# Kernel tuning notes

Measured on AMD Instinct MI355X. Metric: run time of the kernel, lower is better.

The kernel has to match this reference:

```python
import jax, jax.numpy as jnp
import numpy as np

HIDDEN = 2048
INPUT = 2048
BATCH = 4096


def setup_inputs() -> dict:
    key = jax.random.key(0)
    ks = jax.random.split(key, 7)
    x = jax.random.normal(ks[0], (BATCH, INPUT), dtype=jnp.float32)
    h = jax.random.normal(ks[1], (BATCH, HIDDEN), dtype=jnp.float32)
    c = jax.random.normal(ks[2], (BATCH, HIDDEN), dtype=jnp.float32)
    # learned parameters (RandomNormal init stddev=0.05 analogue; scale irrelevant for correctness)
    w_ih = jax.random.normal(ks[3], (4, INPUT, HIDDEN), dtype=jnp.float32) * 0.05
    w_hh = jax.random.normal(ks[4], (4, HIDDEN, HIDDEN), dtype=jnp.float32) * 0.05
    b_ih = jax.random.normal(ks[5], (4, HIDDEN), dtype=jnp.float32) * 0.05
    b_hh = jax.random.normal(ks[6], (4, HIDDEN), dtype=jnp.float32) * 0.05
    return {"x": x, "h": h, "c": c, "w_ih": w_ih, "w_hh": w_hh, "b_ih": b_ih, "b_hh": b_hh}


def reference(x, h, c, w_ih, w_hh, b_ih, b_hh):
    # gates: [4, B, H] = x @ w_ih[g] and h @ w_hh[g], batched over gate dim g
    gates = (
        jnp.einsum("bi,gih->gbh", x, w_ih)
        + jnp.einsum("bh,ghk->gbk", h, w_hh)
        + (b_ih + b_hh)[:, None, :]
    )
    ingate = jax.nn.sigmoid(gates[0])
    forgetgate = jax.nn.sigmoid(gates[1])
    cellgate = jnp.tanh(gates[2])
    outgate = jax.nn.sigmoid(gates[3])
    c_new = forgetgate * c + ingate * cellgate
    h_new = outgate * jnp.tanh(c_new)
    return (h_new, c_new)
```

## Files before the change

kernel.cpp:

```cpp
#include <hip/hip_runtime.h>

#define BATCH  4096
#define HIDDEN 2048
#define INPUT  2048
#define KDIM   4096
#define NDIM   8192
#define BM 128
#define BN 128
#define BK 32

typedef __attribute__((ext_vector_type(8))) short short8;
typedef __attribute__((ext_vector_type(4))) float float4v;


__device__ __forceinline__ unsigned short f2bf(float f) {
    union { float f; unsigned u; } v; v.f = f;
    unsigned r = v.u + 0x7FFFu + ((v.u >> 16) & 1u);
    return (unsigned short)(r >> 16);
}

__device__ __forceinline__ void gl2lds16(const unsigned short* g, unsigned short* l) {
    __builtin_amdgcn_global_load_lds(
        (const __attribute__((address_space(1))) unsigned int*)g,
        (__attribute__((address_space(3))) unsigned int*)l,
        16, 0, 0);
}

__device__ __forceinline__ float sigm(float x) {
    return 1.0f / (1.0f + __expf(-x));
}
__device__ __forceinline__ float tanh_fast(float x) {
    return 2.0f / (1.0f + __expf(-2.0f * x)) - 1.0f;
}


__global__ void pack_x_kernel(const float* __restrict__ x, const float* __restrict__ h,
                              unsigned short* __restrict__ Xb) {
    int idx = blockIdx.x * 256 + threadIdx.x;
    int b  = idx >> 9;
    int ko = idx & 511;
    const float* src = (ko < 256) ? (x + (size_t)b * INPUT  + (size_t)ko * 8)
                                  : (h + (size_t)b * HIDDEN + (size_t)(ko - 256) * 8);
    float4 v0 = *(const float4*)(src);
    float4 v1 = *(const float4*)(src + 4);
    union { unsigned short us[8]; uint4 v; } o;
    o.us[0] = f2bf(v0.x); o.us[1] = f2bf(v0.y); o.us[2] = f2bf(v0.z); o.us[3] = f2bf(v0.w);
    o.us[4] = f2bf(v1.x); o.us[5] = f2bf(v1.y); o.us[6] = f2bf(v1.z); o.us[7] = f2bf(v1.w);
    *(uint4*)(Xb + (size_t)b * KDIM + (size_t)ko * 8) = o.v;
}


__global__ void pack_w_kernel(const float* __restrict__ w_ih, const float* __restrict__ w_hh,
                              unsigned short* __restrict__ Wt) {
    __shared__ unsigned short tile[32][136];
    const int k0 = blockIdx.x * 128;
    const int j0 = blockIdx.y * 32;
    const int g  = blockIdx.z;
    const float* src = (k0 < INPUT)
        ? (w_ih + (size_t)g * INPUT  * HIDDEN + (size_t)k0 * HIDDEN + j0)
        : (w_hh + (size_t)g * HIDDEN * HIDDEN + (size_t)(k0 - INPUT) * HIDDEN + j0);

    const int tid = threadIdx.x;
    const int jl  = (tid & 7) * 4;
    const int kl  = (tid >> 3) * 2;
#pragma unroll
    for (int p = 0; p < 2; ++p) {
        const int k = kl + p * 64;
        float4 v0 = *(const float4*)(src + (size_t)k * HIDDEN + jl);
        float4 v1 = *(const float4*)(src + (size_t)(k + 1) * HIDDEN + jl);
        unsigned p0 = (unsigned)f2bf(v0.x) | ((unsigned)f2bf(v1.x) << 16);
        unsigned p1 = (unsigned)f2bf(v0.y) | ((unsigned)f2bf(v1.y) << 16);
        unsigned p2 = (unsigned)f2bf(v0.z) | ((unsigned)f2bf(v1.z) << 16);
        unsigned p3 = (unsigned)f2bf(v0.w) | ((unsigned)f2bf(v1.w) << 16);
        *(unsigned*)&tile[jl + 0][k] = p0;
        *(unsigned*)&tile[jl + 1][k] = p1;
        *(unsigned*)&tile[jl + 2][k] = p2;
        *(unsigned*)&tile[jl + 3][k] = p3;
    }
    __syncthreads();

#pragma unroll
    for (int p = 0; p < 2; ++p) {
        const int c  = tid + p * 256;
        const int j  = c >> 4;
        const int k8 = c & 15;
        uint4 v = *(const uint4*)&tile[j][k8 * 8];
        *(uint4*)(Wt + (size_t)(4 * (j0 + j) + g) * KDIM + k0 + k8 * 8) = v;
    }
}


__global__ __launch_bounds__(256, 2)
void gemm_kernel(const unsigned short* __restrict__ A,
                 const unsigned short* __restrict__ B,
                 const float* __restrict__ c,
                 const float* __restrict__ b_ih,
                 const float* __restrict__ b_hh,
                 float* __restrict__ out) {
    __shared__ unsigned short As[BM * BK];
    __shared__ unsigned short Bs[BN * BK];

    const int tid  = threadIdx.x;
    const int m0   = blockIdx.y * BM;
    const int n0   = blockIdx.x * BN;
    const int wave = tid >> 6;
    const int lane = tid & 63;
    const int ln   = lane & 15;
    const int kq   = lane >> 4;
    const int wm   = (wave >> 1) * 64;
    const int wn   = (wave & 1) * 64;

    const int s0 = tid, s1 = tid + 256;
    const unsigned short* gA0 = A + (size_t)(m0 + (s0 >> 2)) * KDIM + (s0 & 3) * 8;
    const unsigned short* gA1 = A + (size_t)(m0 + (s1 >> 2)) * KDIM + (s1 & 3) * 8;
    const unsigned short* gB0 = B + (size_t)(n0 + (s0 >> 2)) * KDIM + (s0 & 3) * 8;
    const unsigned short* gB1 = B + (size_t)(n0 + (s1 >> 2)) * KDIM + (s1 & 3) * 8;
    unsigned short* lA0 = As + s0 * 8;
    unsigned short* lA1 = As + s1 * 8;
    unsigned short* lB0 = Bs + s0 * 8;
    unsigned short* lB1 = Bs + s1 * 8;

    float4v acc[4][4];
#pragma unroll
    for (int i = 0; i < 4; ++i)
#pragma unroll
        for (int j = 0; j < 4; ++j)
            acc[i][j] = (float4v){0.f, 0.f, 0.f, 0.f};

    const int a_off = (wm + ln) * BK + kq * 8;
    const int b_off = (wn + ln) * BK + kq * 8;

    for (int kt = 0; kt < KDIM / BK; ++kt) {
        const int ko = kt * BK;
        gl2lds16(gA0 + ko, lA0);
        gl2lds16(gA1 + ko, lA1);
        gl2lds16(gB0 + ko, lB0);
        gl2lds16(gB1 + ko, lB1);
        __syncthreads();

        short8 af[4], bfr[4];
#pragma unroll
        for (int mi = 0; mi < 4; ++mi)
            af[mi] = *(const short8*)(As + a_off + mi * 16 * BK);
#pragma unroll
        for (int ni = 0; ni < 4; ++ni)
            bfr[ni] = *(const short8*)(Bs + b_off + ni * 16 * BK);

#pragma unroll
        for (int mi = 0; mi < 4; ++mi)
#pragma unroll
            for (int ni = 0; ni < 4; ++ni)
                acc[mi][ni] = __builtin_amdgcn_mfma_f32_16x16x32_bf16(
                    af[mi], bfr[ni], acc[mi][ni], 0, 0, 0);

        __syncthreads();
    }

    const int q = lane & 3;
    const int t = (lane & 15) >> 2;
    const size_t HB = (size_t)BATCH * HIDDEN;

#pragma unroll
    for (int ni = 0; ni < 4; ++ni) {
        const int jg = ((n0 + wn + ni * 16) >> 2) + t;
        const float b0 = b_ih[jg]              + b_hh[jg];
        const float b1 = b_ih[HIDDEN + jg]     + b_hh[HIDDEN + jg];
        const float b2 = b_ih[2 * HIDDEN + jg] + b_hh[2 * HIDDEN + jg];
        const float b3 = b_ih[3 * HIDDEN + jg] + b_hh[3 * HIDDEN + jg];
#pragma unroll
        for (int mi = 0; mi < 4; ++mi) {
            float4v v = acc[mi][ni];
            float t1 = __shfl_xor((q & 1) ? v[0] : v[1], 1);
            float t2 = __shfl_xor((q & 1) ? v[2] : v[3], 1);
            v[0] = (q & 1) ? t1 : v[0];
            v[1] = (q & 1) ? v[1] : t1;
            v[2] = (q & 1) ? t2 : v[2];
            v[3] = (q & 1) ? v[3] : t2;
            float t3 = __shfl_xor((q & 2) ? v[0] : v[2], 2);
            float t4 = __shfl_xor((q & 2) ? v[1] : v[3], 2);
            v[0] = (q & 2) ? t3 : v[0];
            v[1] = (q & 2) ? t4 : v[1];
            v[2] = (q & 2) ? v[2] : t3;
            v[3] = (q & 2) ? v[3] : t4;

            const int row = m0 + wm + mi * 16 + kq * 4 + q;
            const float ig = sigm(v[0] + b0);
            const float fg = sigm(v[1] + b1);
            const float cg = tanh_fast(v[2] + b2);
            const float og = sigm(v[3] + b3);
            const float cv = c[(size_t)row * HIDDEN + jg];
            const float cn = fg * cv + ig * cg;
            const float hn = og * tanh_fast(cn);
            out[(size_t)row * HIDDEN + jg] = hn;
            out[HB + (size_t)row * HIDDEN + jg] = cn;
        }
    }
}


extern "C" void kernel_launch(void* const* d_in, const int* in_sizes, int n_in,
                              void* d_out, int out_size, void* d_ws, size_t ws_size,
                              hipStream_t stream) {
    const float* x    = (const float*)d_in[0];
    const float* h    = (const float*)d_in[1];
    const float* c    = (const float*)d_in[2];
    const float* w_ih = (const float*)d_in[3];
    const float* w_hh = (const float*)d_in[4];
    const float* b_ih = (const float*)d_in[5];
    const float* b_hh = (const float*)d_in[6];
    float* out = (float*)d_out;

    const size_t XB_BYTES = (size_t)BATCH * KDIM * 2;
    unsigned short* Xb = (unsigned short*)d_ws;
    unsigned short* Wt = (unsigned short*)((char*)d_ws + XB_BYTES);

    hipLaunchKernelGGL(pack_x_kernel, dim3((size_t)BATCH * KDIM / 8 / 256), dim3(256), 0, stream,
                       x, h, Xb);
    hipLaunchKernelGGL(pack_w_kernel, dim3(KDIM / 128, HIDDEN / 32, 4), dim3(256), 0, stream,
                       w_ih, w_hh, Wt);
    hipLaunchKernelGGL(gemm_kernel, dim3(NDIM / BN, BATCH / BM), dim3(256), 0, stream,
                       Xb, Wt, c, b_ih, b_hh, out);
}
```

Baseline: 565.5 us.

## Enlarge GEMM tiles to 256x256x64 with double-buffered swizzled LDS pipeline

Measured after the change: 512.7 us. -9.3%, faster.

```diff
diff --git a/kernel.cpp b/kernel.cpp
--- a/kernel.cpp
+++ b/kernel.cpp
@@ -5,9 +5,10 @@
 #define INPUT  2048
 #define KDIM   4096
 #define NDIM   8192
-#define BM 128
-#define BN 128
-#define BK 32
+#define BM 256
+#define BN 256
+#define BK 64
+#define NT (KDIM / BK)
 
 typedef __attribute__((ext_vector_type(8))) short short8;
 typedef __attribute__((ext_vector_type(4))) float float4v;
@@ -31,6 +32,12 @@
 }
 __device__ __forceinline__ float tanh_fast(float x) {
     return 2.0f / (1.0f + __expf(-2.0f * x)) - 1.0f;
+}
+
+__device__ __forceinline__ void fence_bar() {
+    asm volatile("" ::: "memory");
+    __builtin_amdgcn_s_barrier();
+    asm volatile("" ::: "memory");
 }
 
 
@@ -81,109 +88,174 @@
 
 #pragma unroll
     for (int p = 0; p < 2; ++p) {
-        const int c  = tid + p * 256;
-        const int j  = c >> 4;
-        const int k8 = c & 15;
+        const int cch = tid + p * 256;
+        const int j   = cch >> 4;
+        const int k8  = cch & 15;
         uint4 v = *(const uint4*)&tile[j][k8 * 8];
         *(uint4*)(Wt + (size_t)(4 * (j0 + j) + g) * KDIM + k0 + k8 * 8) = v;
     }
 }
 
 
-__global__ __launch_bounds__(256, 2)
+__global__ __launch_bounds__(512, 2)
 void gemm_kernel(const unsigned short* __restrict__ A,
                  const unsigned short* __restrict__ B,
                  const float* __restrict__ c,
                  const float* __restrict__ b_ih,
                  const float* __restrict__ b_hh,
                  float* __restrict__ out) {
-    __shared__ unsigned short As[BM * BK];
-    __shared__ unsigned short Bs[BN * BK];
+    extern __shared__ unsigned short lds[];
+    unsigned short* cA = lds;
+    unsigned short* nA = lds + 16384;
+    unsigned short* cB = lds + 32768;
+    unsigned short* nB = lds + 49152;
 
     const int tid  = threadIdx.x;
-    const int m0   = blockIdx.y * BM;
-    const int n0   = blockIdx.x * BN;
-    const int wave = tid >> 6;
+    const int wid  = tid >> 6;
     const int lane = tid & 63;
     const int ln   = lane & 15;
     const int kq   = lane >> 4;
-    const int wm   = (wave >> 1) * 64;
-    const int wn   = (wave & 1) * 64;
-
-    const int s0 = tid, s1 = tid + 256;
-    const unsigned short* gA0 = A + (size_t)(m0 + (s0 >> 2)) * KDIM + (s0 & 3) * 8;
-    const unsigned short* gA1 = A + (size_t)(m0 + (s1 >> 2)) * KDIM + (s1 & 3) * 8;
-    const unsigned short* gB0 = B + (size_t)(n0 + (s0 >> 2)) * KDIM + (s0 & 3) * 8;
-    const unsigned short* gB1 = B + (size_t)(n0 + (s1 >> 2)) * KDIM + (s1 & 3) * 8;
-    unsigned short* lA0 = As + s0 * 8;
-    unsigned short* lA1 = As + s1 * 8;
-    unsigned short* lB0 = Bs + s0 * 8;
-    unsigned short* lB1 = Bs + s1 * 8;
-
-    float4v acc[4][4];
-#pragma unroll
-    for (int i = 0; i < 4; ++i)
+    const int wmr  = (wid >> 2) * 128;
+    const int wnr  = (wid & 3) * 64;
+    const int m0   = blockIdx.y * BM;
+    const int n0   = blockIdx.x * BN;
+
+    const int srow  = tid >> 3;
+    const int scol8 = (tid & 7) ^ (srow & 7);
+    const unsigned short* gA[4];
+    const unsigned short* gB[4];
+#pragma unroll
+    for (int cN = 0; cN < 4; ++cN) {
+        gA[cN] = A + (size_t)(m0 + cN * 64 + srow) * KDIM + scol8 * 8;
+        gB[cN] = B + (size_t)(n0 + cN * 64 + srow) * KDIM + scol8 * 8;
+    }
+    const int dOff = tid * 8;
+
+    const int abase = (wmr + ln) * 64;
+    const int bbase = (wnr + ln) * 64;
+    const int sk0 = ((0 + kq) ^ (ln & 7)) * 8;
+    const int sk1 = ((4 + kq) ^ (ln & 7)) * 8;
+
+    float4v acc[8][4];
+#pragma unroll
+    for (int i = 0; i < 8; ++i)
 #pragma unroll
         for (int j = 0; j < 4; ++j)
             acc[i][j] = (float4v){0.f, 0.f, 0.f, 0.f};
 
-    const int a_off = (wm + ln) * BK + kq * 8;
-    const int b_off = (wn + ln) * BK + kq * 8;
-
-    for (int kt = 0; kt < KDIM / BK; ++kt) {
-        const int ko = kt * BK;
-        gl2lds16(gA0 + ko, lA0);
-        gl2lds16(gA1 + ko, lA1);
-        gl2lds16(gB0 + ko, lB0);
-        gl2lds16(gB1 + ko, lB1);
-        __syncthreads();
-
-        short8 af[4], bfr[4];
-#pragma unroll
-        for (int mi = 0; mi < 4; ++mi)
-            af[mi] = *(const short8*)(As + a_off + mi * 16 * BK);
-#pragma unroll
-        for (int ni = 0; ni < 4; ++ni)
-            bfr[ni] = *(const short8*)(Bs + b_off + ni * 16 * BK);
-
-#pragma unroll
-        for (int mi = 0; mi < 4; ++mi)
-#pragma unroll
-            for (int ni = 0; ni < 4; ++ni)
-                acc[mi][ni] = __builtin_amdgcn_mfma_f32_16x16x32_bf16(
-                    af[mi], bfr[ni], acc[mi][ni], 0, 0, 0);
-
-        __syncthreads();
-    }
-
-    const int q = lane & 3;
-    const int t = (lane & 15) >> 2;
+#define STAGE_A(cN) gl2lds16(gA[cN] + konext, nA + (cN) * 4096 + dOff)
+#define STAGE_B(cN) gl2lds16(gB[cN] + konext, nB + (cN) * 4096 + dOff)
+
+    {
+        const int konext = 0;
+        unsigned short* sA = cA; unsigned short* sB = cB;
+#pragma unroll
+        for (int cN = 0; cN < 4; ++cN) gl2lds16(gB[cN], sB + cN * 4096 + dOff);
+#pragma unroll
+        for (int cN = 0; cN < 4; ++cN) gl2lds16(gA[cN], sA + cN * 4096 + dOff);
+        (void)konext;
+    }
+
+    short8 bf[4][2];
+
+    for (int T = 0; T < NT; ++T) {
+        const bool last = (T == NT - 1);
+        const int konext = (T + 1) * BK;
+
+        if (!last) { STAGE_B(0); STAGE_B(1); }
+        if (!last) asm volatile("s_waitcnt vmcnt(2)" ::: "memory");
+        else       asm volatile("s_waitcnt vmcnt(0)" ::: "memory");
+        fence_bar();
+        {
+#pragma unroll
+            for (int ni = 0; ni < 4; ++ni) {
+                bf[ni][0] = *(const short8*)(cB + bbase + ni * 1024 + sk0);
+                bf[ni][1] = *(const short8*)(cB + bbase + ni * 1024 + sk1);
+            }
+            short8 a00 = *(const short8*)(cA + abase + sk0);
+            short8 a01 = *(const short8*)(cA + abase + sk1);
+            short8 a10 = *(const short8*)(cA + abase + 1024 + sk0);
+            short8 a11 = *(const short8*)(cA + abase + 1024 + sk1);
+            __builtin_amdgcn_s_setprio(1);
+#pragma unroll
+            for (int ni = 0; ni < 4; ++ni)
+                acc[0][ni] = __builtin_amdgcn_mfma_f32_16x16x32_bf16(a00, bf[ni][0], acc[0][ni], 0, 0, 0);
+#pragma unroll
+            for (int ni = 0; ni < 4; ++ni)
+                acc[1][ni] = __builtin_amdgcn_mfma_f32_16x16x32_bf16(a10, bf[ni][0], acc[1][ni], 0, 0, 0);
+#pragma unroll
+            for (int ni = 0; ni < 4; ++ni)
+                acc[0][ni] = __builtin_amdgcn_mfma_f32_16x16x32_bf16(a01, bf[ni][1], acc[0][ni], 0, 0, 0);
+#pragma unroll
+            for (int ni = 0; ni < 4; ++ni)
+                acc[1][ni] = __builtin_amdgcn_mfma_f32_16x16x32_bf16(a11, bf[ni][1], acc[1][ni], 0, 0, 0);
+            __builtin_amdgcn_s_setprio(0);
+        }
+        fence_bar();
+
+#pragma unroll
+        for (int ph = 1; ph < 4; ++ph) {
+            if (!last) {
+                if (ph == 1) { STAGE_B(2); STAGE_B(3); }
+                if (ph == 2) { STAGE_A(0); STAGE_A(2); }
+                if (ph == 3) { STAGE_A(1); STAGE_A(3); }
+            }
+            short8 a00 = *(const short8*)(cA + abase + (2 * ph) * 1024 + sk0);
+            short8 a01 = *(const short8*)(cA + abase + (2 * ph) * 1024 + sk1);
+            short8 a10 = *(const short8*)(cA + abase + (2 * ph + 1) * 1024 + sk0);
+            short8 a11 = *(const short8*)(cA + abase + (2 * ph + 1) * 1024 + sk1);
+            fence_bar();
+            __builtin_amdgcn_s_setprio(1);
+#pragma unroll
+            for (int ni = 0; ni < 4; ++ni)
+                acc[2 * ph][ni] = __builtin_amdgcn_mfma_f32_16x16x32_bf16(a00, bf[ni][0], acc[2 * ph][ni], 0, 0, 0);
+#pragma unroll
+            for (int ni = 0; ni < 4; ++ni)
+                acc[2 * ph + 1][ni] = __builtin_amdgcn_mfma_f32_16x16x32_bf16(a10, bf[ni][0], acc[2 * ph + 1][ni], 0, 0, 0);
+#pragma unroll
+            for (int ni = 0; ni < 4; ++ni)
+                acc[2 * ph][ni] = __builtin_amdgcn_mfma_f32_16x16x32_bf16(a01, bf[ni][1], acc[2 * ph][ni], 0, 0, 0);
+#pragma unroll
+            for (int ni = 0; ni < 4; ++ni)
+                acc[2 * ph + 1][ni] = __builtin_amdgcn_mfma_f32_16x16x32_bf16(a11, bf[ni][1], acc[2 * ph + 1][ni], 0, 0, 0);
+            __builtin_amdgcn_s_setprio(0);
+            fence_bar();
+        }
+
+        unsigned short* t0 = cA; cA = nA; nA = t0;
+        unsigned short* t1 = cB; cB = nB; nB = t1;
+    }
+#undef STAGE_A
+#undef STAGE_B
+
+    const int qg = lane & 3;
+    const int t  = (lane & 15) >> 2;
     const size_t HB = (size_t)BATCH * HIDDEN;
 
 #pragma unroll
     for (int ni = 0; ni < 4; ++ni) {
-        const int jg = ((n0 + wn + ni * 16) >> 2) + t;
+        const int jg = ((n0 + wnr + ni * 16) >> 2) + t;
         const float b0 = b_ih[jg]              + b_hh[jg];
         const float b1 = b_ih[HIDDEN + jg]     + b_hh[HIDDEN + jg];
         const float b2 = b_ih[2 * HIDDEN + jg] + b_hh[2 * HIDDEN + jg];
         const float b3 = b_ih[3 * HIDDEN + jg] + b_hh[3 * HIDDEN + jg];
 #pragma unroll
-        for (int mi = 0; mi < 4; ++mi) {
+        for (int mi = 0; mi < 8; ++mi) {
             float4v v = acc[mi][ni];
-            float t1 = __shfl_xor((q & 1) ? v[0] : v[1], 1);
-            float t2 = __shfl_xor((q & 1) ? v[2] : v[3], 1);
-            v[0] = (q & 1) ? t1 : v[0];
-            v[1] = (q & 1) ? v[1] : t1;
-            v[2] = (q & 1) ? t2 : v[2];
-            v[3] = (q & 1) ? v[3] : t2;
-            float t3 = __shfl_xor((q & 2) ? v[0] : v[2], 2);
-            float t4 = __shfl_xor((q & 2) ? v[1] : v[3], 2);
-            v[0] = (q & 2) ? t3 : v[0];
-            v[1] = (q & 2) ? t4 : v[1];
-            v[2] = (q & 2) ? v[2] : t3;
-            v[3] = (q & 2) ? v[3] : t4;
-
-            const int row = m0 + wm + mi * 16 + kq * 4 + q;
+            float t1 = __shfl_xor((qg & 1) ? v[0] : v[1], 1);
+            float t2 = __shfl_xor((qg & 1) ? v[2] : v[3], 1);
+            v[0] = (qg & 1) ? t1 : v[0];
+            v[1] = (qg & 1) ? v[1] : t1;
+            v[2] = (qg & 1) ? t2 : v[2];
+            v[3] = (qg & 1) ? v[3] : t2;
+            float t3 = __shfl_xor((qg & 2) ? v[0] : v[2], 2);
+            float t4 = __shfl_xor((qg & 2) ? v[1] : v[3], 2);
+            v[0] = (qg & 2) ? t3 : v[0];
+            v[1] = (qg & 2) ? t4 : v[1];
+            v[2] = (qg & 2) ? v[2] : t3;
+            v[3] = (qg & 2) ? v[3] : t4;
+
+            const int row = m0 + wmr + mi * 16 + kq * 4 + qg;
             const float ig = sigm(v[0] + b0);
             const float fg = sigm(v[1] + b1);
             const float cg = tanh_fast(v[2] + b2);
@@ -218,6 +290,6 @@
                        x, h, Xb);
     hipLaunchKernelGGL(pack_w_kernel, dim3(KDIM / 128, HIDDEN / 32, 4), dim3(256), 0, stream,
                        w_ih, w_hh, Wt);
-    hipLaunchKernelGGL(gemm_kernel, dim3(NDIM / BN, BATCH / BM), dim3(256), 0, stream,
+    hipLaunchKernelGGL(gemm_kernel, dim3(NDIM / BN, BATCH / BM), dim3(512), 131072, stream,
                        Xb, Wt, c, b_ih, b_hh, out);
 }
```
